# Kernel tuning notes

Measured on AMD Instinct MI355X. Metric: run time of the kernel, lower is better.

## Reference

```python
import jax, jax.numpy as jnp
import numpy as np

E = 64        # expert_num
H = 64        # expert_hidden_size = hidden_size // expert_num
D_IN = 1024
D_OUT = 1024
T = 65536     # total tokens, pre-sorted by expert; equal groups of T//E


def setup_inputs() -> dict:
    key = jax.random.key(0)
    k1, k2, k3 = jax.random.split(key, 3)
    x = jax.random.normal(k1, (T, D_IN), dtype=jnp.float32)
    batched_fc1_w = jax.random.normal(k2, (E, H, D_IN), dtype=jnp.float32) * 0.02
    batched_fc2_w = jax.random.normal(k3, (E, D_OUT, H), dtype=jnp.float32) * 0.02
    # tokens are sorted by expert; equal-sized groups so sum == T
    fwd_expert_count = jnp.full((E,), T // E, dtype=jnp.int32)
    return {"x": x, "fwd_expert_count": fwd_expert_count,
            "batched_fc1_w": batched_fc1_w, "batched_fc2_w": batched_fc2_w}


def reference(x, fwd_expert_count, batched_fc1_w, batched_fc2_w):
    # Grouped GEMM: tokens are contiguous per expert with fwd_expert_count[e]
    # tokens each. With equal counts this is a fixed-shape batched matmul.
    num_experts = batched_fc1_w.shape[0]
    total = x.shape[0]
    per = total // num_experts
    xg = x.reshape(num_experts, per, -1)              # [E, T/E, d_in]
    h = jnp.einsum('etd,ehd->eth', xg, batched_fc1_w)  # FC1: y = x @ W1^T
    h = jax.nn.relu(h)
    y = jnp.einsum('eth,eoh->eto', h, batched_fc2_w)   # FC2: y = h @ W2^T
    return y.reshape(total, -1)                        # [T, d_out]
```

## Files before the change

### kernel.cpp

```cpp
#include <hip/hip_runtime.h>
#include <hip/hip_bf16.h>

typedef __attribute__((ext_vector_type(4))) float  float4v;
typedef __attribute__((ext_vector_type(4))) short  short4v;
typedef __attribute__((ext_vector_type(8))) short  short8v;
typedef __attribute__((ext_vector_type(8))) __bf16 bf16x8;

constexpr int E_NUM = 64;
constexpr int HID   = 64;
constexpr int DIN   = 1024;
constexpr int DOUT  = 1024;
constexpr int TPE   = 1024;

__device__ __forceinline__ short4v cvt4(float4v v) {
  short4v r;
#pragma unroll
  for (int j = 0; j < 4; j++) {
    __bf16 b = (__bf16)v[j];
    r[j] = __builtin_bit_cast(short, b);
  }
  return r;
}
__device__ __forceinline__ ushort cvt1(float f) {
  __bf16 b = (__bf16)f;
  return __builtin_bit_cast(ushort, b);
}

__global__ __launch_bounds__(512, 4) void fc1_relu_kernel(
    const float* __restrict__ x, const float* __restrict__ w1,
    ushort* __restrict__ hbuf) {
  constexpr int BM = 64, BK = 128;
  __shared__ ushort Xs[2][BM * BK];
  __shared__ ushort Ws[2][HID * BK];

  int nwg = (int)gridDim.x;
  int blk = (int)(blockIdx.x & 7) * (nwg >> 3) + (int)(blockIdx.x >> 3);
  int e  = blk >> 4;
  int rb = blk & 15;
  const float* xe = x  + (size_t)(e * TPE + rb * BM) * DIN;
  const float* we = w1 + (size_t)e * HID * DIN;

  int tid  = (int)threadIdx.x;
  int lane = tid & 63;
  int wv   = tid >> 6;

  float4v xr[4], wr[4];
  int lrow[4];
  int lcol = (lane & 31) * 4;
#pragma unroll
  for (int i = 0; i < 4; i++) lrow[i] = wv * 8 + 2 * i + (lane >> 5);

  auto LOAD = [&](int kt) {
#pragma unroll
    for (int i = 0; i < 4; i++) {
      xr[i] = *(const float4v*)(xe + (size_t)lrow[i] * DIN + kt + lcol);
      wr[i] = *(const float4v*)(we + (size_t)lrow[i] * DIN + kt + lcol);
    }
  };
  auto WRITE = [&](ushort* Xb, ushort* Wb) {
#pragma unroll
    for (int i = 0; i < 4; i++) {
      int r = lrow[i];
      int idx = (r * BK + lcol) ^ ((r & 7) << 3);
      *(short4v*)&Xb[idx] = cvt4(xr[i]);
      *(short4v*)&Wb[idx] = cvt4(wr[i]);
    }
  };

  int m16 = lane & 15;
  int kg  = (lane >> 4) * 8;
  int mf  = wv >> 1;
  int nb2 = (wv & 1) * 2;
  int ar  = mf * 16 + m16;

  float4v acc[2];
#pragma unroll
  for (int j = 0; j < 2; j++)
#pragma unroll
    for (int q = 0; q < 4; q++) acc[j][q] = 0.f;

  auto MMA = [&](const ushort* Xb, const ushort* Wb) {
#pragma unroll
    for (int kk = 0; kk < BK; kk += 32) {
      int k0 = kk + kg;
      short8v a = *(const short8v*)&Xb[(ar * BK + k0) ^ ((ar & 7) << 3)];
#pragma unroll
      for (int j = 0; j < 2; j++) {
        int br = (nb2 + j) * 16 + m16;
        short8v b = *(const short8v*)&Wb[(br * BK + k0) ^ ((br & 7) << 3)];
        acc[j] = __builtin_amdgcn_mfma_f32_16x16x32_bf16(
            __builtin_bit_cast(bf16x8, a), __builtin_bit_cast(bf16x8, b),
            acc[j], 0, 0, 0);
      }
    }
  };

  LOAD(0);
#pragma unroll
  for (int s = 0; s < 8; s++) {
    int buf = s & 1;
    WRITE(Xs[buf], Ws[buf]);
    __syncthreads();
    if (s < 7) LOAD((s + 1) * BK);
    MMA(Xs[buf], Ws[buf]);
  }

  ushort* hs = &Xs[0][0];
#pragma unroll
  for (int j = 0; j < 2; j++) {
    int col = (nb2 + j) * 16 + m16;
#pragma unroll
    for (int q = 0; q < 4; q++) {
      int row = mf * 16 + ((lane >> 4) << 2) + q;
      hs[row * HID + col] = cvt1(fmaxf(acc[j][q], 0.f));
    }
  }
  __syncthreads();
  size_t rowbase = (size_t)e * TPE + rb * BM;
  int row = tid >> 3, c8 = (tid & 7) * 8;
  short8v v = *(const short8v*)&hs[row * HID + c8];
  *(short8v*)(hbuf + (rowbase + row) * HID + c8) = v;
}

__global__ __launch_bounds__(256) void fc2_kernel(
    const ushort* __restrict__ hbuf, const float* __restrict__ w2,
    float* __restrict__ y) {
  constexpr int BM = 128, BN = 128, K = 64;
  __shared__ __align__(16) ushort smem[BM * K + BN * K];
  ushort* Hs = smem;
  ushort* Ws = smem + BM * K;

  int nwg = (int)gridDim.x;
  int blk = (int)(blockIdx.x & 7) * (nwg >> 3) + (int)(blockIdx.x >> 3);

  int e  = blk >> 6;
  int mb = (blk >> 3) & 7;
  int nb = blk & 7;
  const ushort* he = hbuf + (size_t)(e * TPE + mb * BM) * K;
  const float*  we = w2 + ((size_t)e * DOUT + nb * BN) * K;

  int tid  = (int)threadIdx.x;
  int lane = tid & 63;
  int wv   = tid >> 6;

#pragma unroll
  for (int i = 0; i < 4; i++) {
    int f = tid + i * 256;
    int row = f >> 3, c8 = f & 7;
    short8v v = *(const short8v*)(he + (size_t)row * K + c8 * 8);
    *(short8v*)&Hs[(row * K + c8 * 8) ^ ((row & 7) << 3)] = v;
  }
#pragma unroll
  for (int i = 0; i < 8; i++) {
    int f = tid + i * 256;
    int row = f >> 4, c4 = f & 15;
    float4v v = *(const float4v*)(we + (size_t)row * K + c4 * 4);
    *(short4v*)&Ws[(row * K + c4 * 4) ^ ((row & 7) << 3)] = cvt4(v);
  }
  __syncthreads();

  float4v acc[2][8];
#pragma unroll
  for (int mf = 0; mf < 2; mf++)
#pragma unroll
    for (int nf = 0; nf < 8; nf++)
#pragma unroll
      for (int j = 0; j < 4; j++) acc[mf][nf][j] = 0.f;

  int kg = (lane >> 4) * 8;
#pragma unroll
  for (int kk = 0; kk < K; kk += 32) {
    int k0 = kk + kg;
    short8v a[2];
#pragma unroll
    for (int mf = 0; mf < 2; mf++) {
      int arr = wv * 32 + mf * 16 + (lane & 15);
      a[mf] = *(const short8v*)&Hs[(arr * K + k0) ^ ((arr & 7) << 3)];
    }
#pragma unroll
    for (int nf = 0; nf < 8; nf++) {
      int br = nf * 16 + (lane & 15);
      short8v b = *(const short8v*)&Ws[(br * K + k0) ^ ((br & 7) << 3)];
#pragma unroll
      for (int mf = 0; mf < 2; mf++)
        acc[mf][nf] = __builtin_amdgcn_mfma_f32_16x16x32_bf16(
            __builtin_bit_cast(bf16x8, a[mf]), __builtin_bit_cast(bf16x8, b),
            acc[mf][nf], 0, 0, 0);
    }
  }

  float* Yt = (float*)smem;
  size_t rowbase = (size_t)(e * TPE + mb * BM);
  int col0 = nb * BN;
#pragma unroll
  for (int pass = 0; pass < 2; pass++) {
    __syncthreads();
    if ((wv >> 1) == pass) {
      int lrow0 = (wv & 1) * 32;
#pragma unroll
      for (int mf = 0; mf < 2; mf++) {
#pragma unroll
        for (int j = 0; j < 4; j++) {
          int lrow = lrow0 + mf * 16 + ((lane >> 4) << 2) + j;
#pragma unroll
          for (int nf = 0; nf < 8; nf++)
            Yt[lrow * BN + nf * 16 + (lane & 15)] = acc[mf][nf][j];
        }
      }
    }
    __syncthreads();
#pragma unroll
    for (int i = 0; i < 8; i++) {
      int idx  = tid + i * 256;
      int lrow = idx >> 5;
      int c4   = idx & 31;
      float4v v = *(const float4v*)&Yt[lrow * BN + c4 * 4];
      float* dst = y + (rowbase + pass * 64 + lrow) * DOUT + col0 + c4 * 4;
      __builtin_nontemporal_store(v, (float4v*)dst);
    }
  }
}

extern "C" void kernel_launch(void* const* d_in, const int* in_sizes, int n_in,
                              void* d_out, int out_size, void* d_ws, size_t ws_size,
                              hipStream_t stream) {
  const float* x  = (const float*)d_in[0];
  const float* w1 = (const float*)d_in[2];
  const float* w2 = (const float*)d_in[3];
  float* yout = (float*)d_out;
  ushort* hbuf = (ushort*)d_ws;

  fc1_relu_kernel<<<E_NUM * 16, 512, 0, stream>>>(x, w1, hbuf);
  fc2_kernel<<<E_NUM * 64, 256, 0, stream>>>(hbuf, w2, yout);
}
```

Baseline: 111.2 us.

## Halve FC1 K-tile and raise occupancy with 8-wide swizzled LDS writes

FC1 K-tile shrinks from 128 to 64, which halves LDS use and cuts the per-thread prefetch registers from eight float4 to four, so launch bounds can ask for 6 blocks per CU instead of 4. Each thread now loads 8 contiguous floats per row and writes one 16-byte bf16 chunk to LDS. The XOR swizzle is applied at chunk granularity on both the write and the MFMA reads. The cost is twice as many K iterations and barriers.

```diff
diff --git a/kernel.cpp b/kernel.cpp
--- a/kernel.cpp
+++ b/kernel.cpp
@@ -26,10 +26,10 @@
   return __builtin_bit_cast(ushort, b);
 }
 
-__global__ __launch_bounds__(512, 4) void fc1_relu_kernel(
+__global__ __launch_bounds__(512, 6) void fc1_relu_kernel(
     const float* __restrict__ x, const float* __restrict__ w1,
     ushort* __restrict__ hbuf) {
-  constexpr int BM = 64, BK = 128;
+  constexpr int BM = 64, BK = 64;
   __shared__ ushort Xs[2][BM * BK];
   __shared__ ushort Ws[2][HID * BK];
 
@@ -44,27 +44,31 @@
   int lane = tid & 63;
   int wv   = tid >> 6;
 
-  float4v xr[4], wr[4];
-  int lrow[4];
-  int lcol = (lane & 31) * 4;
-#pragma unroll
-  for (int i = 0; i < 4; i++) lrow[i] = wv * 8 + 2 * i + (lane >> 5);
-
+  int row_s = wv * 8 + (lane >> 3);
+  int s8    = lane & 7;
+  int ul    = s8 ^ (row_s & 7);
+  int lidx  = row_s * BK + ul * 8;
+
+  float4v xlo, xhi, wlo, whi;
   auto LOAD = [&](int kt) {
-#pragma unroll
-    for (int i = 0; i < 4; i++) {
-      xr[i] = *(const float4v*)(xe + (size_t)lrow[i] * DIN + kt + lcol);
-      wr[i] = *(const float4v*)(we + (size_t)lrow[i] * DIN + kt + lcol);
-    }
+    const float* px = xe + (size_t)row_s * DIN + kt + s8 * 8;
+    const float* pw = we + (size_t)row_s * DIN + kt + s8 * 8;
+    xlo = *(const float4v*)(px);
+    xhi = *(const float4v*)(px + 4);
+    wlo = *(const float4v*)(pw);
+    whi = *(const float4v*)(pw + 4);
   };
   auto WRITE = [&](ushort* Xb, ushort* Wb) {
-#pragma unroll
-    for (int i = 0; i < 4; i++) {
-      int r = lrow[i];
-      int idx = (r * BK + lcol) ^ ((r & 7) << 3);
-      *(short4v*)&Xb[idx] = cvt4(xr[i]);
-      *(short4v*)&Wb[idx] = cvt4(wr[i]);
-    }
+    short4v a0 = cvt4(xlo), a1 = cvt4(xhi);
+    short4v b0 = cvt4(wlo), b1 = cvt4(whi);
+    short8v xa, wb;
+#pragma unroll
+    for (int q = 0; q < 4; q++) {
+      xa[q] = a0[q]; xa[q + 4] = a1[q];
+      wb[q] = b0[q]; wb[q + 4] = b1[q];
+    }
+    *(short8v*)&Xb[lidx] = xa;
+    *(short8v*)&Wb[lidx] = wb;
   };
 
   int m16 = lane & 15;
@@ -82,12 +86,12 @@
   auto MMA = [&](const ushort* Xb, const ushort* Wb) {
 #pragma unroll
     for (int kk = 0; kk < BK; kk += 32) {
-      int k0 = kk + kg;
-      short8v a = *(const short8v*)&Xb[(ar * BK + k0) ^ ((ar & 7) << 3)];
+      int c = (kk + kg) >> 3;
+      short8v a = *(const short8v*)&Xb[ar * BK + (c ^ (ar & 7)) * 8];
 #pragma unroll
       for (int j = 0; j < 2; j++) {
         int br = (nb2 + j) * 16 + m16;
-        short8v b = *(const short8v*)&Wb[(br * BK + k0) ^ ((br & 7) << 3)];
+        short8v b = *(const short8v*)&Wb[br * BK + (c ^ (br & 7)) * 8];
         acc[j] = __builtin_amdgcn_mfma_f32_16x16x32_bf16(
             __builtin_bit_cast(bf16x8, a), __builtin_bit_cast(bf16x8, b),
             acc[j], 0, 0, 0);
@@ -97,11 +101,11 @@
 
   LOAD(0);
 #pragma unroll
-  for (int s = 0; s < 8; s++) {
+  for (int s = 0; s < 16; s++) {
     int buf = s & 1;
     WRITE(Xs[buf], Ws[buf]);
     __syncthreads();
-    if (s < 7) LOAD((s + 1) * BK);
+    if (s < 15) LOAD((s + 1) * BK);
     MMA(Xs[buf], Ws[buf]);
   }
 
```

After: 117.3 us. 5.5% more time.
